# Performance work log

Measured on AMD Instinct MI355X. Metric: run time of the kernel, lower is better.

The kernel has to match this reference:

```python
import jax, jax.numpy as jnp
import numpy as np

PAD = 1  # PAD_token; embedding rows at PAD are zero (padding_idx)


def setup_inputs() -> dict:
    V, D, HOPS = 50000, 128, 3
    B, Lc, Mc = 16, 256, 8
    Lk, Mk = 512, 8
    key = jax.random.key(0)
    kC, kK, kc, kk = jax.random.split(key, 4)
    # one table per hop (C_0..C_{HOPS-1}, K_0..K_{HOPS-1}), init N(0, 0.1)
    C = 0.1 * jax.random.normal(kC, (HOPS, V, D), dtype=jnp.float32)
    K = 0.1 * jax.random.normal(kK, (HOPS, V, D), dtype=jnp.float32)
    C = C.at[:, PAD].set(0.0)
    K = K.at[:, PAD].set(0.0)
    conv_seqs = jax.random.randint(kc, (B, Lc, Mc), 0, V)
    kb_arr = jax.random.randint(kk, (B, Lk, Mk), 0, V)  # dense, PAD-padded ragged KB
    return {"conv_seqs": conv_seqs, "kb_arr": kb_arr, "C": C, "K": K}


def reference(conv_seqs, kb_arr, C, K):
    B, Lc, _ = conv_seqs.shape
    HOPS, _, D = C.shape
    conv_feature = jnp.zeros((B, Lc, D), dtype=C.dtype)
    for hop in range(HOPS):
        # embedding-bag: gather + sum over span tokens
        cf = jnp.sum(C[hop][conv_seqs], axis=2)  # [B, Lc, D]
        kf = jnp.sum(K[hop][kb_arr], axis=2)     # [B, Lk, D]
        att = jnp.einsum('bld,bkd->blk', cf, kf)  # [B, Lc, Lk]
        p = jax.nn.softmax(att, axis=-1)
        conv_feature = jnp.einsum('blk,bkd->bld', p, kf) + conv_feature
    return conv_feature.transpose(1, 0, 2)  # [Lc, B, D]
```

## Files before the change

### kernel.cpp

```cpp
#include <hip/hip_runtime.h>

#define V_    50000
#define D_    128
#define HOPS_ 3
#define B_    16
#define LC_   256
#define MC_   8
#define LK_   512
#define MK_   8

typedef __bf16  bf16x8  __attribute__((ext_vector_type(8)));
typedef unsigned short ushort8 __attribute__((ext_vector_type(8)));
typedef unsigned short ushort4v __attribute__((ext_vector_type(4)));
typedef float   floatx4 __attribute__((ext_vector_type(4)));

__device__ inline unsigned short f2bf(float f) {
    union { float f; unsigned u; } x; x.f = f;
    unsigned r = x.u + 0x7FFFu + ((x.u >> 16) & 1u);
    return (unsigned short)(r >> 16);
}

__device__ inline floatx4 mfma_bf16(ushort8 a, ushort8 b, floatx4 c) {
    return __builtin_amdgcn_mfma_f32_16x16x32_bf16(
        __builtin_bit_cast(bf16x8, a), __builtin_bit_cast(bf16x8, b), c, 0, 0, 0);
}

__global__ __launch_bounds__(256, 7) void gather_kernel(
    const int* __restrict__ conv_seqs, const int* __restrict__ kb_arr,
    const float* __restrict__ Ct, const float* __restrict__ Kt,
    unsigned short* __restrict__ kf, unsigned short* __restrict__ kfT,
    unsigned short* __restrict__ cf, float4* __restrict__ out4)
{
    __shared__ unsigned short tile[32][132];

    const int tid  = threadIdx.x;
    const int bx   = blockIdx.x;

    constexpr int KBLK = HOPS_ * B_ * (LK_ / 32);
    constexpr int CBLK = HOPS_ * B_ * (LC_ / 32);

    if (bx >= KBLK + CBLK) {
        out4[(size_t)(bx - (KBLK + CBLK)) * 256 + tid] =
            make_float4(0.f, 0.f, 0.f, 0.f);
        return;
    }

    const int r    = tid >> 3;
    const int s    = tid & 7;
    const int lane = tid & 63;

    const int*   idxp;
    const float* table;
    unsigned short* dst;
    bool do_transpose;
    int g, row0;

    if (bx < KBLK) {
        int hop  = bx / (B_ * 16);
        int rem  = bx % (B_ * 16);
        int b    = rem >> 4;
        row0 = (rem & 15) * 32;
        g    = hop * B_ + b;
        idxp  = kb_arr + (size_t)(b * LK_ + row0 + r) * MK_;
        table = Kt + (size_t)hop * V_ * D_;
        dst   = kf + ((size_t)g * LK_ + row0 + r) * D_;
        do_transpose = true;
    } else {
        int id   = bx - KBLK;
        int hop  = id / (B_ * 8);
        int rem  = id % (B_ * 8);
        int b    = rem >> 3;
        row0 = (rem & 7) * 32;
        g    = hop * B_ + b;
        idxp  = conv_seqs + (size_t)(b * LC_ + row0 + r) * MC_;
        table = Ct + (size_t)hop * V_ * D_;
        dst   = cf + ((size_t)g * LC_ + row0 + r) * D_;
        do_transpose = false;
    }

    const int myidx = idxp[s];
    int idxs[8];
    #pragma unroll
    for (int m = 0; m < 8; ++m)
        idxs[m] = __shfl(myidx, (lane & 56) + m);

    float4 acc[4];
    #pragma unroll
    for (int j = 0; j < 4; ++j) acc[j] = make_float4(0.f, 0.f, 0.f, 0.f);

    #pragma unroll
    for (int m = 0; m < 8; ++m) {
        const float* rowp = table + (size_t)idxs[m] * D_;
        #pragma unroll
        for (int j = 0; j < 4; ++j) {
            float4 v = *(const float4*)(rowp + j * 32 + s * 4);
            acc[j].x += v.x; acc[j].y += v.y; acc[j].z += v.z; acc[j].w += v.w;
        }
    }

    ushort4v o[4];
    #pragma unroll
    for (int j = 0; j < 4; ++j) {
        o[j][0] = f2bf(acc[j].x); o[j][1] = f2bf(acc[j].y);
        o[j][2] = f2bf(acc[j].z); o[j][3] = f2bf(acc[j].w);
        *(ushort4v*)(dst + j * 32 + s * 4) = o[j];
    }

    if (do_transpose) {
        #pragma unroll
        for (int j = 0; j < 4; ++j)
            *(ushort4v*)&tile[r][j * 32 + s * 4] = o[j];
        __syncthreads();
        const int d    = tid >> 1;
        const int half = tid & 1;
        unsigned short* tdst =
            kfT + ((size_t)g * D_ + d) * LK_ + row0 + half * 16;
        ushort8 a, b;
        #pragma unroll
        for (int i = 0; i < 8; ++i) a[i] = tile[half * 16 + i][d];
        #pragma unroll
        for (int i = 0; i < 8; ++i) b[i] = tile[half * 16 + 8 + i][d];
        *(ushort8*)(tdst)     = a;
        *(ushort8*)(tdst + 8) = b;
    }
}

__global__ __launch_bounds__(512) void attn_kernel(
    const unsigned short* __restrict__ kf, const unsigned short* __restrict__ kfT,
    const unsigned short* __restrict__ cf, float* __restrict__ out)
{
    constexpr int AS = 516;
    constexpr int PS = 520;
    __shared__ float att_s[16][AS];
    __shared__ unsigned short p_s[16][PS];
    __shared__ float rowinv_s[16];

    const int tid  = threadIdx.x;
    const int wave = tid >> 6;
    const int lane = tid & 63;
    const int quad = lane >> 4;
    const int l16  = lane & 15;

    const int gl  = blockIdx.x & 7;
    const int s_  = blockIdx.x >> 3;
    const int lt  = s_ / 6;
    const int gh  = s_ % 6;
    const int g   = gh * 8 + gl;
    const int b   = g & 15;
    const int l0  = lt * 16;

    const unsigned short* cf_h  = cf  + (((size_t)g) * 256 + l0) * 128;
    const unsigned short* kf_h  = kf  + ((size_t)g) * 512 * 128;
    const unsigned short* kfT_h = kfT + ((size_t)g) * 128 * 512;

    ushort8 afrag[4];
    #pragma unroll
    for (int ks = 0; ks < 4; ++ks)
        afrag[ks] = *(const ushort8*)(cf_h + l16 * 128 + ks * 32 + quad * 8);

    #pragma unroll
    for (int t = 0; t < 4; ++t) {
        const int nt = wave * 4 + t;
        floatx4 acc = {0.f, 0.f, 0.f, 0.f};
        #pragma unroll
        for (int ks = 0; ks < 4; ++ks) {
            ushort8 bfrag = *(const ushort8*)(kf_h + (nt * 16 + l16) * 128 + ks * 32 + quad * 8);
            acc = mfma_bf16(afrag[ks], bfrag, acc);
        }
        #pragma unroll
        for (int rr = 0; rr < 4; ++rr)
            att_s[quad * 4 + rr][nt * 16 + l16] = acc[rr];
    }
    __syncthreads();

    #pragma unroll
    for (int rr = 0; rr < 2; ++rr) {
        const int row = wave * 2 + rr;
        float v[8];
        float mx = -1e30f;
        #pragma unroll
        for (int j = 0; j < 8; ++j) {
            v[j] = att_s[row][lane + j * 64];
            mx = fmaxf(mx, v[j]);
        }
        #pragma unroll
        for (int off = 32; off; off >>= 1) mx = fmaxf(mx, __shfl_xor(mx, off));
        float sum = 0.f;
        #pragma unroll
        for (int j = 0; j < 8; ++j) {
            float e = __expf(v[j] - mx);
            p_s[row][lane + j * 64] = f2bf(e);
            sum += e;
        }
        #pragma unroll
        for (int off = 32; off; off >>= 1) sum += __shfl_xor(sum, off);
        if (lane == 0) rowinv_s[row] = 1.0f / sum;
    }
    __syncthreads();

    floatx4 pacc = {0.f, 0.f, 0.f, 0.f};
    #pragma unroll
    for (int ks = 0; ks < 16; ++ks) {
        ushort8 pa    = *(const ushort8*)&p_s[l16][ks * 32 + quad * 8];
        ushort8 bfrag = *(const ushort8*)(kfT_h + (size_t)(wave * 16 + l16) * 512 + ks * 32 + quad * 8);
        pacc = mfma_bf16(pa, bfrag, pacc);
    }

    const int d = wave * 16 + l16;
    #pragma unroll
    for (int rr = 0; rr < 4; ++rr)
        atomicAdd(&out[(((size_t)(l0 + quad * 4 + rr)) * 16 + b) * 128 + d],
                  pacc[rr] * rowinv_s[quad * 4 + rr]);
}

extern "C" void kernel_launch(void* const* d_in, const int* in_sizes, int n_in,
                              void* d_out, int out_size, void* d_ws, size_t ws_size,
                              hipStream_t stream) {
    (void)in_sizes; (void)n_in; (void)out_size; (void)ws_size;
    const int*   conv_seqs = (const int*)d_in[0];
    const int*   kb_arr    = (const int*)d_in[1];
    const float* C         = (const float*)d_in[2];
    const float* K         = (const float*)d_in[3];

    unsigned short* kf  = (unsigned short*)d_ws;
    unsigned short* kfT = kf  + (size_t)HOPS_ * B_ * LK_ * D_;
    unsigned short* cf  = kfT + (size_t)HOPS_ * B_ * LK_ * D_;
    float* out = (float*)d_out;

    hipLaunchKernelGGL(gather_kernel, dim3(1664), dim3(256), 0, stream,
                       conv_seqs, kb_arr, C, K, kf, kfT, cf, (float4*)out);
    hipLaunchKernelGGL(attn_kernel, dim3(768), dim3(512), 0, stream,
                       kf, kfT, cf, out);
}
```

Before: 190.5 us.

## Fuse conv embedding-bag gather into attention kernel and shrink K-gather tiles

The conversation-side embedding-bag sum moves out of the gather kernel and into the attention kernel. Each attention block gathers its 16 query rows straight into shared memory, reusing the p_s buffer, so cf is no longer written to and read back from a global workspace. The K gather kernel now uses 16-row tiles with 16 threads per row and 8 columns each, which gives more blocks and a smaller transpose tile. The cost is extra latency at the start of each attention block from the random table reads.

```diff
diff --git a/kernel.cpp b/kernel.cpp
--- a/kernel.cpp
+++ b/kernel.cpp
@@ -25,109 +25,75 @@
         __builtin_bit_cast(bf16x8, a), __builtin_bit_cast(bf16x8, b), c, 0, 0, 0);
 }
 
-__global__ __launch_bounds__(256, 7) void gather_kernel(
-    const int* __restrict__ conv_seqs, const int* __restrict__ kb_arr,
-    const float* __restrict__ Ct, const float* __restrict__ Kt,
+__global__ __launch_bounds__(256, 6) void gather_kernel(
+    const int* __restrict__ kb_arr, const float* __restrict__ Kt,
     unsigned short* __restrict__ kf, unsigned short* __restrict__ kfT,
-    unsigned short* __restrict__ cf, float4* __restrict__ out4)
+    float4* __restrict__ out4)
 {
-    __shared__ unsigned short tile[32][132];
+    __shared__ unsigned short tile[16][136];
 
     const int tid  = threadIdx.x;
     const int bx   = blockIdx.x;
 
-    constexpr int KBLK = HOPS_ * B_ * (LK_ / 32);
-    constexpr int CBLK = HOPS_ * B_ * (LC_ / 32);
-
-    if (bx >= KBLK + CBLK) {
-        out4[(size_t)(bx - (KBLK + CBLK)) * 256 + tid] =
-            make_float4(0.f, 0.f, 0.f, 0.f);
+    constexpr int KBLK = HOPS_ * B_ * (LK_ / 16);
+
+    if (bx >= KBLK) {
+        out4[(size_t)(bx - KBLK) * 256 + tid] = make_float4(0.f, 0.f, 0.f, 0.f);
         return;
     }
 
-    const int r    = tid >> 3;
-    const int s    = tid & 7;
+    const int r    = tid >> 4;
+    const int s    = tid & 15;
     const int lane = tid & 63;
 
-    const int*   idxp;
-    const float* table;
-    unsigned short* dst;
-    bool do_transpose;
-    int g, row0;
-
-    if (bx < KBLK) {
-        int hop  = bx / (B_ * 16);
-        int rem  = bx % (B_ * 16);
-        int b    = rem >> 4;
-        row0 = (rem & 15) * 32;
-        g    = hop * B_ + b;
-        idxp  = kb_arr + (size_t)(b * LK_ + row0 + r) * MK_;
-        table = Kt + (size_t)hop * V_ * D_;
-        dst   = kf + ((size_t)g * LK_ + row0 + r) * D_;
-        do_transpose = true;
-    } else {
-        int id   = bx - KBLK;
-        int hop  = id / (B_ * 8);
-        int rem  = id % (B_ * 8);
-        int b    = rem >> 3;
-        row0 = (rem & 7) * 32;
-        g    = hop * B_ + b;
-        idxp  = conv_seqs + (size_t)(b * LC_ + row0 + r) * MC_;
-        table = Ct + (size_t)hop * V_ * D_;
-        dst   = cf + ((size_t)g * LC_ + row0 + r) * D_;
-        do_transpose = false;
-    }
-
-    const int myidx = idxp[s];
+    const int hop  = bx / (B_ * 32);
+    const int rem  = bx % (B_ * 32);
+    const int b    = rem >> 5;
+    const int row0 = (rem & 31) * 16;
+    const int g    = hop * B_ + b;
+
+    const int* idxp = kb_arr + (size_t)(b * LK_ + row0 + r) * MK_;
+    const float* table = Kt + (size_t)hop * V_ * D_;
+    unsigned short* dst = kf + ((size_t)g * LK_ + row0 + r) * D_;
+
+    const int myidx = idxp[s & 7];
     int idxs[8];
     #pragma unroll
     for (int m = 0; m < 8; ++m)
-        idxs[m] = __shfl(myidx, (lane & 56) + m);
-
-    float4 acc[4];
-    #pragma unroll
-    for (int j = 0; j < 4; ++j) acc[j] = make_float4(0.f, 0.f, 0.f, 0.f);
+        idxs[m] = __shfl(myidx, (lane & 48) + m);
+
+    float4 a0 = make_float4(0.f, 0.f, 0.f, 0.f);
+    float4 a1 = make_float4(0.f, 0.f, 0.f, 0.f);
 
     #pragma unroll
     for (int m = 0; m < 8; ++m) {
-        const float* rowp = table + (size_t)idxs[m] * D_;
-        #pragma unroll
-        for (int j = 0; j < 4; ++j) {
-            float4 v = *(const float4*)(rowp + j * 32 + s * 4);
-            acc[j].x += v.x; acc[j].y += v.y; acc[j].z += v.z; acc[j].w += v.w;
-        }
-    }
-
-    ushort4v o[4];
-    #pragma unroll
-    for (int j = 0; j < 4; ++j) {
-        o[j][0] = f2bf(acc[j].x); o[j][1] = f2bf(acc[j].y);
-        o[j][2] = f2bf(acc[j].z); o[j][3] = f2bf(acc[j].w);
-        *(ushort4v*)(dst + j * 32 + s * 4) = o[j];
-    }
-
-    if (do_transpose) {
-        #pragma unroll
-        for (int j = 0; j < 4; ++j)
-            *(ushort4v*)&tile[r][j * 32 + s * 4] = o[j];
-        __syncthreads();
-        const int d    = tid >> 1;
-        const int half = tid & 1;
-        unsigned short* tdst =
-            kfT + ((size_t)g * D_ + d) * LK_ + row0 + half * 16;
-        ushort8 a, b;
-        #pragma unroll
-        for (int i = 0; i < 8; ++i) a[i] = tile[half * 16 + i][d];
-        #pragma unroll
-        for (int i = 0; i < 8; ++i) b[i] = tile[half * 16 + 8 + i][d];
-        *(ushort8*)(tdst)     = a;
-        *(ushort8*)(tdst + 8) = b;
-    }
+        const float4* rowp = (const float4*)(table + (size_t)idxs[m] * D_);
+        float4 v0 = rowp[s * 2];
+        float4 v1 = rowp[s * 2 + 1];
+        a0.x += v0.x; a0.y += v0.y; a0.z += v0.z; a0.w += v0.w;
+        a1.x += v1.x; a1.y += v1.y; a1.z += v1.z; a1.w += v1.w;
+    }
+
+    ushort8 o;
+    o[0] = f2bf(a0.x); o[1] = f2bf(a0.y); o[2] = f2bf(a0.z); o[3] = f2bf(a0.w);
+    o[4] = f2bf(a1.x); o[5] = f2bf(a1.y); o[6] = f2bf(a1.z); o[7] = f2bf(a1.w);
+    *(ushort8*)(dst + s * 8) = o;
+
+    *(ushort8*)&tile[r][s * 8] = o;
+    __syncthreads();
+    const int d    = tid >> 1;
+    const int half = tid & 1;
+    unsigned short* tdst = kfT + ((size_t)g * D_ + d) * LK_ + row0 + half * 8;
+    ushort8 t8;
+    #pragma unroll
+    for (int i = 0; i < 8; ++i) t8[i] = tile[half * 8 + i][d];
+    *(ushort8*)(tdst) = t8;
 }
 
 __global__ __launch_bounds__(512) void attn_kernel(
+    const int* __restrict__ conv_seqs, const float* __restrict__ Ct,
     const unsigned short* __restrict__ kf, const unsigned short* __restrict__ kfT,
-    const unsigned short* __restrict__ cf, float* __restrict__ out)
+    float* __restrict__ out)
 {
     constexpr int AS = 516;
     constexpr int PS = 520;
@@ -135,6 +101,8 @@
     __shared__ unsigned short p_s[16][PS];
     __shared__ float rowinv_s[16];
 
+    unsigned short* cf_s = &p_s[0][0];
+
     const int tid  = threadIdx.x;
     const int wave = tid >> 6;
     const int lane = tid & 63;
@@ -146,17 +114,36 @@
     const int lt  = s_ / 6;
     const int gh  = s_ % 6;
     const int g   = gh * 8 + gl;
+    const int hop = g >> 4;
     const int b   = g & 15;
     const int l0  = lt * 16;
 
-    const unsigned short* cf_h  = cf  + (((size_t)g) * 256 + l0) * 128;
     const unsigned short* kf_h  = kf  + ((size_t)g) * 512 * 128;
     const unsigned short* kfT_h = kfT + ((size_t)g) * 128 * 512;
 
+    {
+        const int bag = tid >> 5;
+        const int sl  = tid & 31;
+        const int d0  = sl * 4;
+        const int* idxp = conv_seqs + (size_t)(b * LC_ + l0 + bag) * MC_;
+        const float* table = Ct + (size_t)hop * V_ * D_;
+        float4 acc = make_float4(0.f, 0.f, 0.f, 0.f);
+        #pragma unroll
+        for (int m = 0; m < 8; ++m) {
+            const float4 v = *(const float4*)(table + (size_t)idxp[m] * D_ + d0);
+            acc.x += v.x; acc.y += v.y; acc.z += v.z; acc.w += v.w;
+        }
+        ushort4v oc;
+        oc[0] = f2bf(acc.x); oc[1] = f2bf(acc.y);
+        oc[2] = f2bf(acc.z); oc[3] = f2bf(acc.w);
+        *(ushort4v*)&cf_s[bag * 132 + d0] = oc;
+    }
+    __syncthreads();
+
     ushort8 afrag[4];
     #pragma unroll
     for (int ks = 0; ks < 4; ++ks)
-        afrag[ks] = *(const ushort8*)(cf_h + l16 * 128 + ks * 32 + quad * 8);
+        afrag[ks] = *(const ushort8*)&cf_s[l16 * 132 + ks * 32 + quad * 8];
 
     #pragma unroll
     for (int t = 0; t < 4; ++t) {
@@ -223,12 +210,11 @@
     const float* K         = (const float*)d_in[3];
 
     unsigned short* kf  = (unsigned short*)d_ws;
-    unsigned short* kfT = kf  + (size_t)HOPS_ * B_ * LK_ * D_;
-    unsigned short* cf  = kfT + (size_t)HOPS_ * B_ * LK_ * D_;
+    unsigned short* kfT = kf + (size_t)HOPS_ * B_ * LK_ * D_;
     float* out = (float*)d_out;
 
-    hipLaunchKernelGGL(gather_kernel, dim3(1664), dim3(256), 0, stream,
-                       conv_seqs, kb_arr, C, K, kf, kfT, cf, (float4*)out);
+    hipLaunchKernelGGL(gather_kernel, dim3(2048), dim3(256), 0, stream,
+                       kb_arr, K, kf, kfT, (float4*)out);
     hipLaunchKernelGGL(attn_kernel, dim3(768), dim3(512), 0, stream,
-                       kf, kfT, cf, out);
-}
+                       conv_seqs, C, kf, kfT, out);
+}
```

New measurement: 189.1 us. About the same (-0.7%).
